# Kernel tuning notes

Hardware: AMD Instinct MI355X
Metric: run time of the kernel (lower is better)

Reference implementation:

```python
import jax, jax.numpy as jnp
import numpy as np

N = 100000      # nodes
E = 1600000     # edges
F = 92          # raw node feature length
H = 128         # element_embedding == hidden_encoding (GatedGraphConv out_channels)
STEPS = 6       # mpnn_steps
G = 256         # graphs in batch


def setup_inputs() -> dict:
    key = jax.random.key(0)
    ks = jax.random.split(key, 10)
    s = 0.05
    x = jax.random.normal(ks[0], (N, F), dtype=jnp.float32)
    edge_index = jax.random.randint(ks[1], (2, E), 0, N, dtype=jnp.int64)
    batch = jnp.sort(jax.random.randint(ks[2], (N,), 0, G, dtype=jnp.int64))
    # atom_input: Linear(F, H, bias=False); applied as x @ W_embed with W_embed [F, H]
    W_embed = jax.random.normal(ks[3], (F, H), dtype=jnp.float32) * s
    # GatedGraphConv weight: [num_layers, H, H], used as h @ W_mpnn[i]
    W_mpnn = jax.random.normal(ks[4], (STEPS, H, H), dtype=jnp.float32) * s
    # torch.nn.GRUCell params: weight_ih/hh [3H, H], bias_ih/hh [3H]
    w_ih = jax.random.normal(ks[5], (3 * H, H), dtype=jnp.float32) * s
    w_hh = jax.random.normal(ks[6], (3 * H, H), dtype=jnp.float32) * s
    b_ih = jax.random.normal(ks[7], (3 * H,), dtype=jnp.float32) * s
    b_hh = jax.random.normal(ks[8], (3 * H,), dtype=jnp.float32) * s
    # prediction_layer: Linear(H, 1)
    w_pred = jax.random.normal(ks[9], (H, 1), dtype=jnp.float32) * s
    b_pred = jnp.zeros((1,), dtype=jnp.float32)
    return {"x": x, "edge_index": edge_index, "batch": batch,
            "W_embed": W_embed, "W_mpnn": W_mpnn,
            "w_ih": w_ih, "w_hh": w_hh, "b_ih": b_ih, "b_hh": b_hh,
            "w_pred": w_pred, "b_pred": b_pred}


def reference(x, edge_index, batch, W_embed, W_mpnn, w_ih, w_hh, b_ih, b_hh, w_pred, b_pred):
    n = x.shape[0]
    src, dst = edge_index[0], edge_index[1]  # PyG: messages flow source -> target
    # atom_input (no bias) + tanh; element_embedding == H so no zero-padding needed
    h = jnp.tanh(x @ W_embed)  # [N, H]

    def step(h, W):
        m = h @ W                                             # per-step linear [N, H]
        agg = jax.ops.segment_sum(m[src], dst, num_segments=n)  # scatter-add aggr
        # torch GRUCell(input=agg, hidden=h)
        gi = agg @ w_ih.T + b_ih                              # [N, 3H]
        gh = h @ w_hh.T + b_hh                                # [N, 3H]
        i_r, i_z, i_n = jnp.split(gi, 3, axis=-1)
        h_r, h_z, h_n = jnp.split(gh, 3, axis=-1)
        r = jax.nn.sigmoid(i_r + h_r)
        z = jax.nn.sigmoid(i_z + h_z)
        cand = jnp.tanh(i_n + r * h_n)
        h_new = (1.0 - z) * cand + z * h
        return h_new, None

    h, _ = jax.lax.scan(step, h, W_mpnn)

    # global_mean_pool over graph ids
    sums = jax.ops.segment_sum(h, batch, num_segments=G)                           # [G, H]
    counts = jax.ops.segment_sum(jnp.ones((n, 1), h.dtype), batch, num_segments=G)  # [G, 1]
    pooled = sums / jnp.maximum(counts, 1.0)
    pooled = jax.nn.relu(pooled)
    return (pooled @ w_pred + b_pred)[:, 0]  # [G]
```

## Files before the change

### kernel.cpp

```cpp
#include <hip/hip_runtime.h>
#include <math.h>

#define N_NODES 100000
#define N_PAD   100032
#define N_EDGES 1600000
#define F_IN    92
#define H_DIM   128
#define STEPS   6
#define G_GRAPHS 256
#define TH3     384
#define SSTR    136
#define HSTR    132
#define FPASS   8
#define FRANGE  12500

typedef __attribute__((ext_vector_type(8))) short bf16x8;
typedef __attribute__((ext_vector_type(4))) float f32x4;

__device__ __forceinline__ unsigned short f2bf(float x) {
    unsigned u = __float_as_uint(x);
    return (unsigned short)((u + 0x7fffu + ((u >> 16) & 1u)) >> 16);
}
__device__ __forceinline__ float bf2f(unsigned short h) {
    return __uint_as_float(((unsigned)h) << 16);
}

__global__ void fuse_w_kernel(const float* __restrict__ Wm, const float* __restrict__ w_ih,
                              float* __restrict__ M2) {
    int ij = blockIdx.x;
    int i  = ij / TH3;
    int j  = ij - i * TH3;
    int k  = threadIdx.x;
    __shared__ float wj[H_DIM];
    wj[k] = w_ih[j * H_DIM + k];
    __syncthreads();
    const float* wr = Wm + ((size_t)i * H_DIM + k) * H_DIM;
    float acc = 0.f;
    #pragma unroll 4
    for (int c = 0; c < H_DIM; ++c) acc = fmaf(wj[c], wr[c], acc);
    M2[((size_t)i * TH3 + j) * H_DIM + k] = acc;
}

__global__ void pack_kernel(const float* __restrict__ M6, const float* __restrict__ w_hh,
                            unsigned short* __restrict__ PBhi, unsigned short* __restrict__ PBlo) {
    int b    = blockIdx.x;
    int lane = threadIdx.x;
    int kc   = b & 3;
    int ct   = (b >> 2) & 7;
    int mg   = b >> 5;
    int g    = mg % 3;
    int mat  = mg / 3;
    int j    = g * 128 + ct * 16 + (lane & 15);
    int k0   = kc * 32 + (lane >> 4) * 8;
    size_t outBase = ((size_t)b * 64 + lane) * 8;
    #pragma unroll
    for (int jj = 0; jj < 8; ++jj) {
        int k = k0 + jj;
        float v = (mat < 6) ? M6[((size_t)mat * TH3 + j) * H_DIM + k]
                            : w_hh[(size_t)j * H_DIM + k];
        unsigned short hv = f2bf(v);
        PBhi[outBase + jj] = hv;
        PBlo[outBase + jj] = f2bf(v - bf2f(hv));
    }
}

#define ET 16
__global__ void embed_kernel(const float* __restrict__ x, const float* __restrict__ We,
                             unsigned short* __restrict__ h_hi, unsigned short* __restrict__ h_lo) {
    int n0 = blockIdx.x * ET;
    int j  = threadIdx.x;
    __shared__ float xs[ET * F_IN];
    for (int i = j; i < ET * F_IN; i += H_DIM) xs[i] = x[n0 * F_IN + i];
    __syncthreads();
    float acc[ET];
    #pragma unroll
    for (int n = 0; n < ET; ++n) acc[n] = 0.f;
    const float4* xs4 = (const float4*)xs;
    for (int k4 = 0; k4 < F_IN / 4; ++k4) {
        int k = k4 * 4;
        float w0 = We[(k + 0) * H_DIM + j];
        float w1 = We[(k + 1) * H_DIM + j];
        float w2 = We[(k + 2) * H_DIM + j];
        float w3 = We[(k + 3) * H_DIM + j];
        #pragma unroll
        for (int n = 0; n < ET; ++n) {
            float4 a = xs4[n * (F_IN / 4) + k4];
            acc[n] = fmaf(a.x, w0, acc[n]);
            acc[n] = fmaf(a.y, w1, acc[n]);
            acc[n] = fmaf(a.z, w2, acc[n]);
            acc[n] = fmaf(a.w, w3, acc[n]);
        }
    }
    #pragma unroll
    for (int n = 0; n < ET; ++n) {
        float e2 = __expf(2.f * acc[n]);
        float v  = 1.f - 2.f / (e2 + 1.f);
        size_t o = (size_t)(n0 + n) * H_DIM + j;
        unsigned short hv = f2bf(v);
        h_hi[o] = hv;
        h_lo[o] = f2bf(v - bf2f(hv));
    }
}

__global__ void hist_kernel(const int* __restrict__ dst, int* __restrict__ count) {
    int e = blockIdx.x * 256 + threadIdx.x;
    if (e < N_EDGES) atomicAdd(&count[dst[e]], 1);
}

__global__ void scan_block_kernel(const int* __restrict__ count, int* __restrict__ offs,
                                  int* __restrict__ blockSums) {
    __shared__ int tmp[256];
    int i = blockIdx.x * 256 + threadIdx.x;
    int t = threadIdx.x;
    int v = (i < N_NODES) ? count[i] : 0;
    tmp[t] = v;
    __syncthreads();
    for (int d = 1; d < 256; d <<= 1) {
        int add = (t >= d) ? tmp[t - d] : 0;
        __syncthreads();
        tmp[t] += add;
        __syncthreads();
    }
    if (i < N_NODES) offs[i] = tmp[t] - v;
    if (t == 255) blockSums[blockIdx.x] = tmp[255];
}

__global__ void scan_sums_kernel(int* __restrict__ blockSums, int nb) {
    __shared__ int tmp[512];
    int t = threadIdx.x;
    int v = (t < nb) ? blockSums[t] : 0;
    tmp[t] = v;
    __syncthreads();
    for (int d = 1; d < 512; d <<= 1) {
        int add = (t >= d) ? tmp[t - d] : 0;
        __syncthreads();
        tmp[t] += add;
        __syncthreads();
    }
    if (t < nb) blockSums[t] = tmp[t] - v;
}

__global__ void scan_add_kernel(int* __restrict__ offs, const int* __restrict__ blockSums) {
    int i = blockIdx.x * 256 + threadIdx.x;
    if (i < N_NODES) offs[i] += blockSums[blockIdx.x];
    if (i == 0) offs[N_NODES] = N_EDGES;
}

__global__ void fill_kernel(const int* __restrict__ src, const int* __restrict__ dst,
                            const int* __restrict__ offs, int* __restrict__ cursor,
                            int* __restrict__ srcSorted) {
    int e = blockIdx.x * 256 + threadIdx.x;
    if (e >= N_EDGES) return;
    for (int p = 0; p < FPASS; ++p) {
        int lo = p * FRANGE;
        int d = dst[e];
        if (d >= lo && d < lo + FRANGE) {
            int pos = atomicAdd(&cursor[d], 1);
            srcSorted[offs[d] + pos] = src[e];
        }
    }
}

__global__ void gather_kernel(const unsigned short* __restrict__ h_hi,
                              const int* __restrict__ offs, const int* __restrict__ srcS,
                              unsigned short* __restrict__ sv) {
    int tid  = blockIdx.x * 256 + threadIdx.x;
    int node = tid >> 4;
    int c8   = (tid & 15) * 8;
    float a[8];
    #pragma unroll
    for (int j = 0; j < 8; ++j) a[j] = 0.f;
    if (node < N_NODES) {
        int beg = offs[node], end = offs[node + 1];
        int i = beg;
        for (; i + 4 <= end; i += 4) {
            int n0 = srcS[i], n1 = srcS[i + 1], n2 = srcS[i + 2], n3 = srcS[i + 3];
            bf16x8 v0 = *(const bf16x8*)(h_hi + (size_t)n0 * H_DIM + c8);
            bf16x8 v1 = *(const bf16x8*)(h_hi + (size_t)n1 * H_DIM + c8);
            bf16x8 v2 = *(const bf16x8*)(h_hi + (size_t)n2 * H_DIM + c8);
            bf16x8 v3 = *(const bf16x8*)(h_hi + (size_t)n3 * H_DIM + c8);
            #pragma unroll
            for (int j = 0; j < 8; ++j)
                a[j] += (bf2f((unsigned short)v0[j]) + bf2f((unsigned short)v1[j]))
                      + (bf2f((unsigned short)v2[j]) + bf2f((unsigned short)v3[j]));
        }
        if (i + 2 <= end) {
            int n0 = srcS[i], n1 = srcS[i + 1];
            bf16x8 v0 = *(const bf16x8*)(h_hi + (size_t)n0 * H_DIM + c8);
            bf16x8 v1 = *(const bf16x8*)(h_hi + (size_t)n1 * H_DIM + c8);
            #pragma unroll
            for (int j = 0; j < 8; ++j)
                a[j] += bf2f((unsigned short)v0[j]) + bf2f((unsigned short)v1[j]);
            i += 2;
        }
        if (i < end) {
            int n0 = srcS[i];
            bf16x8 v0 = *(const bf16x8*)(h_hi + (size_t)n0 * H_DIM + c8);
            #pragma unroll
            for (int j = 0; j < 8; ++j) a[j] += bf2f((unsigned short)v0[j]);
        }
    }
    bf16x8 o;
    #pragma unroll
    for (int j = 0; j < 8; ++j) o[j] = (short)f2bf(a[j]);
    *(bf16x8*)(sv + (size_t)node * H_DIM + c8) = o;
}

__global__ __launch_bounds__(512, 2) void gru_kernel(
    const unsigned short* __restrict__ sv,
    unsigned short* __restrict__ h_hi, unsigned short* __restrict__ h_lo,
    const unsigned short* __restrict__ PBhi, const unsigned short* __restrict__ PBlo,
    int matI, const float* __restrict__ b_ih, const float* __restrict__ b_hh)
{
    __shared__ __align__(16) unsigned short buf[3 * 64 * SSTR];
    unsigned short* sS  = buf;
    unsigned short* sHh = buf + 64 * SSTR;
    unsigned short* sHl = buf + 2 * 64 * SSTR;
    float* hnF = (float*)buf;

    int nt = blockIdx.x;
    int rowBase = nt * 64;
    int t = threadIdx.x;

    #pragma unroll
    for (int i = t; i < 64 * 16; i += 512) {
        int row = i >> 4;
        int c8  = (i & 15) * 8;
        size_t g = (size_t)(rowBase + row) * H_DIM + c8;
        int l = row * SSTR + c8;
        *(bf16x8*)&sS [l] = *(const bf16x8*)(sv   + g);
        *(bf16x8*)&sHh[l] = *(const bf16x8*)(h_hi + g);
        *(bf16x8*)&sHl[l] = *(const bf16x8*)(h_lo + g);
    }
    __syncthreads();

    int lane = t & 63;
    int ct   = t >> 6;
    int rloc = lane & 15;
    int kOff = (lane >> 4) * 8;

    f32x4 accI[3][4], accH[3][4];
    #pragma unroll
    for (int g = 0; g < 3; ++g)
        #pragma unroll
        for (int rs = 0; rs < 4; ++rs) {
            accI[g][rs] = (f32x4){0.f, 0.f, 0.f, 0.f};
            accH[g][rs] = (f32x4){0.f, 0.f, 0.f, 0.f};
        }

    const int fI0 = matI * 3;
    for (int kc = 0; kc < 4; ++kc) {
        int aOff = kc * 32 + kOff;
        bf16x8 aS[4];
        #pragma unroll
        for (int rs = 0; rs < 4; ++rs)
            aS[rs] = *(const bf16x8*)(&sS[(rs * 16 + rloc) * SSTR + aOff]);
        #pragma unroll
        for (int g = 0; g < 3; ++g) {
            size_t oI = ((size_t)((fI0 + g) * 32 + ct * 4 + kc) * 64 + lane) * 8;
            bf16x8 bh = *(const bf16x8*)(PBhi + oI);
            bf16x8 bl = *(const bf16x8*)(PBlo + oI);
            #pragma unroll
            for (int rs = 0; rs < 4; ++rs) {
                accI[g][rs] = __builtin_amdgcn_mfma_f32_16x16x32_bf16(aS[rs], bh, accI[g][rs], 0, 0, 0);
                accI[g][rs] = __builtin_amdgcn_mfma_f32_16x16x32_bf16(aS[rs], bl, accI[g][rs], 0, 0, 0);
            }
        }
        bf16x8 aHh4[4], aHl4[4];
        #pragma unroll
        for (int rs = 0; rs < 4; ++rs) {
            int al = (rs * 16 + rloc) * SSTR + aOff;
            aHh4[rs] = *(const bf16x8*)(&sHh[al]);
            aHl4[rs] = *(const bf16x8*)(&sHl[al]);
        }
        #pragma unroll
        for (int g = 0; g < 3; ++g) {
            size_t oH = ((size_t)((18 + g) * 32 + ct * 4 + kc) * 64 + lane) * 8;
            bf16x8 bh = *(const bf16x8*)(PBhi + oH);
            bf16x8 bl = *(const bf16x8*)(PBlo + oH);
            #pragma unroll
            for (int rs = 0; rs < 4; ++rs) {
                accH[g][rs] = __builtin_amdgcn_mfma_f32_16x16x32_bf16(aHh4[rs], bh, accH[g][rs], 0, 0, 0);
                accH[g][rs] = __builtin_amdgcn_mfma_f32_16x16x32_bf16(aHl4[rs], bh, accH[g][rs], 0, 0, 0);
                accH[g][rs] = __builtin_amdgcn_mfma_f32_16x16x32_bf16(aHh4[rs], bl, accH[g][rs], 0, 0, 0);
            }
        }
    }

    int c = ct * 16 + rloc;
    float bir = b_ih[c], biz = b_ih[128 + c], bin = b_ih[256 + c];
    float bhr = b_hh[c], bhz = b_hh[128 + c], bhn = b_hh[256 + c];
    int rl = (lane >> 4) * 4;

    float hnv[4][4];
    #pragma unroll
    for (int rs = 0; rs < 4; ++rs) {
        #pragma unroll
        for (int r = 0; r < 4; ++r) {
            int lrow = rs * 16 + rl + r;
            float hold = bf2f(sHh[lrow * SSTR + c]) + bf2f(sHl[lrow * SSTR + c]);
            float gr = (accI[0][rs][r] + bir) + (accH[0][rs][r] + bhr);
            float gz = (accI[1][rs][r] + biz) + (accH[1][rs][r] + bhz);
            float rr = 1.f / (1.f + __expf(-gr));
            float zz = 1.f / (1.f + __expf(-gz));
            float pre = (accI[2][rs][r] + bin) + rr * (accH[2][rs][r] + bhn);
            float e2 = __expf(2.f * pre);
            float cand = 1.f - 2.f / (e2 + 1.f);
            hnv[rs][r] = (1.f - zz) * cand + zz * hold;
        }
    }
    __syncthreads();
    #pragma unroll
    for (int rs = 0; rs < 4; ++rs)
        #pragma unroll
        for (int r = 0; r < 4; ++r)
            hnF[(rs * 16 + rl + r) * HSTR + c] = hnv[rs][r];
    __syncthreads();
    #pragma unroll
    for (int i = t; i < 64 * 32; i += 512) {
        int row = i >> 5;
        int c4  = (i & 31) * 4;
        int gRow = rowBase + row;
        if (gRow < N_NODES) {
            float4 v = *(const float4*)(&hnF[row * HSTR + c4]);
            ushort4 hh, ll;
            hh.x = f2bf(v.x); ll.x = f2bf(v.x - bf2f(hh.x));
            hh.y = f2bf(v.y); ll.y = f2bf(v.y - bf2f(hh.y));
            hh.z = f2bf(v.z); ll.z = f2bf(v.z - bf2f(hh.z));
            hh.w = f2bf(v.w); ll.w = f2bf(v.w - bf2f(hh.w));
            size_t o = (size_t)gRow * H_DIM + c4;
            *(ushort4*)(h_hi + o) = hh;
            *(ushort4*)(h_lo + o) = ll;
        }
    }
}

__global__ void pool_partial(const unsigned short* __restrict__ h_hi,
                             const unsigned short* __restrict__ h_lo,
                             const int* __restrict__ batch,
                             float* __restrict__ pooled) {
    int b = blockIdx.x;
    int t = threadIdx.x;
    int n0 = b * 64;
    if (n0 >= N_NODES) return;
    int nEnd = n0 + 64 < N_NODES ? n0 + 64 : N_NODES;
    int curG = batch[n0];
    float acc = 0.f;
    for (int n = n0; n < nEnd; ++n) {
        int g = batch[n];
        if (g != curG) {
            atomicAdd(&pooled[curG * H_DIM + t], acc);
            acc = 0.f;
            curG = g;
        }
        size_t o = (size_t)n * H_DIM + t;
        acc += bf2f(h_hi[o]) + bf2f(h_lo[o]);
    }
    atomicAdd(&pooled[curG * H_DIM + t], acc);
}

__global__ void pool_head(const float* __restrict__ pooled, const int* __restrict__ batch,
                          const float* __restrict__ w_pred, const float* __restrict__ b_pred,
                          float* __restrict__ out) {
    int g = blockIdx.x;
    int t = threadIdx.x;
    __shared__ int bounds[2];
    __shared__ float red[2];
    if (t < 2) {
        int target = g + t;
        int lo = 0, hi = N_NODES;
        while (lo < hi) {
            int mid = (lo + hi) >> 1;
            if (batch[mid] < target) lo = mid + 1; else hi = mid;
        }
        bounds[t] = lo;
    }
    __syncthreads();
    int cnt = bounds[1] - bounds[0];
    float pv = pooled[g * H_DIM + t] / fmaxf((float)cnt, 1.f);
    pv = fmaxf(pv, 0.f);
    float v = pv * w_pred[t];
    #pragma unroll
    for (int off = 32; off > 0; off >>= 1) v += __shfl_down(v, off);
    if ((t & 63) == 0) red[t >> 6] = v;
    __syncthreads();
    if (t == 0) out[g] = red[0] + red[1] + b_pred[0];
}

extern "C" void kernel_launch(void* const* d_in, const int* in_sizes, int n_in,
                              void* d_out, int out_size, void* d_ws, size_t ws_size,
                              hipStream_t stream) {
    const float* x      = (const float*)d_in[0];
    const int*   ei     = (const int*)d_in[1];
    const int*   batch  = (const int*)d_in[2];
    const float* We     = (const float*)d_in[3];
    const float* Wm     = (const float*)d_in[4];
    const float* w_ih   = (const float*)d_in[5];
    const float* w_hh   = (const float*)d_in[6];
    const float* b_ih   = (const float*)d_in[7];
    const float* b_hh   = (const float*)d_in[8];
    const float* w_pred = (const float*)d_in[9];
    const float* b_pred = (const float*)d_in[10];
    float* out = (float*)d_out;

    const size_t HN = (size_t)N_PAD * H_DIM;
    unsigned short* h_hi = (unsigned short*)d_ws;
    unsigned short* h_lo = h_hi + HN;
    unsigned short* sv   = h_lo + HN;
    float* M6 = (float*)(sv + HN);
    unsigned short* PBhi = (unsigned short*)(M6 + (size_t)STEPS * TH3 * H_DIM);
    unsigned short* PBlo = PBhi + 21 * 32 * 64 * 8;
    int* offs      = (int*)(PBlo + 21 * 32 * 64 * 8);
    int* srcSorted = offs + (N_NODES + 1);
    float* pooled  = (float*)(srcSorted + N_EDGES);
    int* count     = (int*)sv;
    int* cursor    = count + N_NODES;
    int* blockSums = cursor + N_NODES;

    const int* esrc = ei;
    const int* edst = ei + N_EDGES;
    const int EB = (N_EDGES + 255) / 256;
    const int NB = (N_NODES + 255) / 256;

    hipMemsetAsync(count, 0, 2 * (size_t)N_NODES * sizeof(int), stream);
    hipMemsetAsync(pooled, 0, (size_t)G_GRAPHS * H_DIM * sizeof(float), stream);
    hist_kernel<<<EB, 256, 0, stream>>>(edst, count);
    scan_block_kernel<<<NB, 256, 0, stream>>>(count, offs, blockSums);
    scan_sums_kernel<<<1, 512, 0, stream>>>(blockSums, NB);
    scan_add_kernel<<<NB, 256, 0, stream>>>(offs, blockSums);
    fill_kernel<<<EB, 256, 0, stream>>>(esrc, edst, offs, cursor, srcSorted);

    fuse_w_kernel<<<STEPS * TH3, H_DIM, 0, stream>>>(Wm, w_ih, M6);
    pack_kernel<<<21 * 32, 64, 0, stream>>>(M6, w_hh, PBhi, PBlo);
    embed_kernel<<<N_NODES / ET, H_DIM, 0, stream>>>(x, We, h_hi, h_lo);

    for (int i = 0; i < STEPS; ++i) {
        gather_kernel<<<(N_PAD * 16) / 256, 256, 0, stream>>>(h_hi, offs, srcSorted, sv);
        gru_kernel<<<N_PAD / 64, 512, 0, stream>>>(sv, h_hi, h_lo, PBhi, PBlo,
                                                   i, b_ih, b_hh);
    }

    pool_partial<<<N_PAD / 64, H_DIM, 0, stream>>>(h_hi, h_lo, batch, pooled);
    pool_head<<<G_GRAPHS, H_DIM, 0, stream>>>(pooled, batch, w_pred, b_pred, out);
}
```

Before: 1.211 ms.

## Merge r/z accumulators, load agg operand from global, raise GRU occupancy

After: 1.459 ms. +20.5%, slower.

```diff
diff --git a/kernel.cpp b/kernel.cpp
--- a/kernel.cpp
+++ b/kernel.cpp
@@ -206,16 +206,15 @@
     *(bf16x8*)(sv + (size_t)node * H_DIM + c8) = o;
 }
 
-__global__ __launch_bounds__(512, 2) void gru_kernel(
+__global__ __launch_bounds__(512, 4) void gru_kernel(
     const unsigned short* __restrict__ sv,
     unsigned short* __restrict__ h_hi, unsigned short* __restrict__ h_lo,
     const unsigned short* __restrict__ PBhi, const unsigned short* __restrict__ PBlo,
     int matI, const float* __restrict__ b_ih, const float* __restrict__ b_hh)
 {
-    __shared__ __align__(16) unsigned short buf[3 * 64 * SSTR];
-    unsigned short* sS  = buf;
-    unsigned short* sHh = buf + 64 * SSTR;
-    unsigned short* sHl = buf + 2 * 64 * SSTR;
+    __shared__ __align__(16) unsigned short buf[2 * 64 * SSTR];
+    unsigned short* sHh = buf;
+    unsigned short* sHl = buf + 64 * SSTR;
     float* hnF = (float*)buf;
 
     int nt = blockIdx.x;
@@ -228,7 +227,6 @@
         int c8  = (i & 15) * 8;
         size_t g = (size_t)(rowBase + row) * H_DIM + c8;
         int l = row * SSTR + c8;
-        *(bf16x8*)&sS [l] = *(const bf16x8*)(sv   + g);
         *(bf16x8*)&sHh[l] = *(const bf16x8*)(h_hi + g);
         *(bf16x8*)&sHl[l] = *(const bf16x8*)(h_lo + g);
     }
@@ -239,14 +237,14 @@
     int rloc = lane & 15;
     int kOff = (lane >> 4) * 8;
 
-    f32x4 accI[3][4], accH[3][4];
-    #pragma unroll
-    for (int g = 0; g < 3; ++g)
-        #pragma unroll
-        for (int rs = 0; rs < 4; ++rs) {
-            accI[g][rs] = (f32x4){0.f, 0.f, 0.f, 0.f};
-            accH[g][rs] = (f32x4){0.f, 0.f, 0.f, 0.f};
-        }
+    f32x4 accRZ[2][4], accIn[4], accHn[4];
+    #pragma unroll
+    for (int rs = 0; rs < 4; ++rs) {
+        accRZ[0][rs] = (f32x4){0.f, 0.f, 0.f, 0.f};
+        accRZ[1][rs] = (f32x4){0.f, 0.f, 0.f, 0.f};
+        accIn[rs]    = (f32x4){0.f, 0.f, 0.f, 0.f};
+        accHn[rs]    = (f32x4){0.f, 0.f, 0.f, 0.f};
+    }
 
     const int fI0 = matI * 3;
     for (int kc = 0; kc < 4; ++kc) {
@@ -254,18 +252,7 @@
         bf16x8 aS[4];
         #pragma unroll
         for (int rs = 0; rs < 4; ++rs)
-            aS[rs] = *(const bf16x8*)(&sS[(rs * 16 + rloc) * SSTR + aOff]);
-        #pragma unroll
-        for (int g = 0; g < 3; ++g) {
-            size_t oI = ((size_t)((fI0 + g) * 32 + ct * 4 + kc) * 64 + lane) * 8;
-            bf16x8 bh = *(const bf16x8*)(PBhi + oI);
-            bf16x8 bl = *(const bf16x8*)(PBlo + oI);
-            #pragma unroll
-            for (int rs = 0; rs < 4; ++rs) {
-                accI[g][rs] = __builtin_amdgcn_mfma_f32_16x16x32_bf16(aS[rs], bh, accI[g][rs], 0, 0, 0);
-                accI[g][rs] = __builtin_amdgcn_mfma_f32_16x16x32_bf16(aS[rs], bl, accI[g][rs], 0, 0, 0);
-            }
-        }
+            aS[rs] = *(const bf16x8*)(sv + (size_t)(rowBase + rs * 16 + rloc) * H_DIM + aOff);
         bf16x8 aHh4[4], aHl4[4];
         #pragma unroll
         for (int rs = 0; rs < 4; ++rs) {
@@ -275,21 +262,29 @@
         }
         #pragma unroll
         for (int g = 0; g < 3; ++g) {
-            size_t oH = ((size_t)((18 + g) * 32 + ct * 4 + kc) * 64 + lane) * 8;
-            bf16x8 bh = *(const bf16x8*)(PBhi + oH);
-            bf16x8 bl = *(const bf16x8*)(PBlo + oH);
+            size_t oI = ((size_t)((fI0 + g) * 32 + ct * 4 + kc) * 64 + lane) * 8;
+            size_t oH = ((size_t)((18  + g) * 32 + ct * 4 + kc) * 64 + lane) * 8;
+            bf16x8 bIh = *(const bf16x8*)(PBhi + oI);
+            bf16x8 bIl = *(const bf16x8*)(PBlo + oI);
+            bf16x8 bHh = *(const bf16x8*)(PBhi + oH);
+            bf16x8 bHl = *(const bf16x8*)(PBlo + oH);
             #pragma unroll
             for (int rs = 0; rs < 4; ++rs) {
-                accH[g][rs] = __builtin_amdgcn_mfma_f32_16x16x32_bf16(aHh4[rs], bh, accH[g][rs], 0, 0, 0);
-                accH[g][rs] = __builtin_amdgcn_mfma_f32_16x16x32_bf16(aHl4[rs], bh, accH[g][rs], 0, 0, 0);
-                accH[g][rs] = __builtin_amdgcn_mfma_f32_16x16x32_bf16(aHh4[rs], bl, accH[g][rs], 0, 0, 0);
+                f32x4* tI = (g == 0) ? &accRZ[0][rs] : (g == 1) ? &accRZ[1][rs] : &accIn[rs];
+                f32x4* tH = (g == 2) ? &accHn[rs] : tI;
+                *tI = __builtin_amdgcn_mfma_f32_16x16x32_bf16(aS[rs],   bIh, *tI, 0, 0, 0);
+                *tI = __builtin_amdgcn_mfma_f32_16x16x32_bf16(aS[rs],   bIl, *tI, 0, 0, 0);
+                *tH = __builtin_amdgcn_mfma_f32_16x16x32_bf16(aHh4[rs], bHh, *tH, 0, 0, 0);
+                *tH = __builtin_amdgcn_mfma_f32_16x16x32_bf16(aHl4[rs], bHh, *tH, 0, 0, 0);
+                *tH = __builtin_amdgcn_mfma_f32_16x16x32_bf16(aHh4[rs], bHl, *tH, 0, 0, 0);
             }
         }
     }
 
     int c = ct * 16 + rloc;
-    float bir = b_ih[c], biz = b_ih[128 + c], bin = b_ih[256 + c];
-    float bhr = b_hh[c], bhz = b_hh[128 + c], bhn = b_hh[256 + c];
+    float br  = b_ih[c] + b_hh[c];
+    float bz  = b_ih[128 + c] + b_hh[128 + c];
+    float bin = b_ih[256 + c], bhn = b_hh[256 + c];
     int rl = (lane >> 4) * 4;
 
     float hnv[4][4];
@@ -299,11 +294,9 @@
         for (int r = 0; r < 4; ++r) {
             int lrow = rs * 16 + rl + r;
             float hold = bf2f(sHh[lrow * SSTR + c]) + bf2f(sHl[lrow * SSTR + c]);
-            float gr = (accI[0][rs][r] + bir) + (accH[0][rs][r] + bhr);
-            float gz = (accI[1][rs][r] + biz) + (accH[1][rs][r] + bhz);
-            float rr = 1.f / (1.f + __expf(-gr));
-            float zz = 1.f / (1.f + __expf(-gz));
-            float pre = (accI[2][rs][r] + bin) + rr * (accH[2][rs][r] + bhn);
+            float rr = 1.f / (1.f + __expf(-(accRZ[0][rs][r] + br)));
+            float zz = 1.f / (1.f + __expf(-(accRZ[1][rs][r] + bz)));
+            float pre = (accIn[rs][r] + bin) + rr * (accHn[rs][r] + bhn);
             float e2 = __expf(2.f * pre);
             float cand = 1.f - 2.f / (e2 + 1.f);
             hnv[rs][r] = (1.f - zz) * cand + zz * hold;
```
